# Kernel optimization log

Measured on AMD Instinct MI355X. Metric: run time of the kernel, lower is better.

Reference implementation:

```python
import jax, jax.numpy as jnp
import numpy as np

H, I, E, TOP_K = 2048, 5632, 8, 2


def _silu_mul_mlp(x, w_gate_up, w_down):
    # x: [T,H], w_gate_up: [H,2I], w_down: [I,H]
    gu = x @ w_gate_up
    g, u = jnp.split(gu, 2, axis=-1)
    return (jax.nn.silu(g) * u) @ w_down


def setup_inputs() -> dict:
    key = jax.random.key(0)
    ks = jax.random.split(key, 6)
    s = 0.02  # init scale for weights
    x = jax.random.normal(ks[0], (2, 1024, H), jnp.float32)
    gate_w = jax.random.normal(ks[1], (E, H), jnp.float32) * s
    base_gate_up = jax.random.normal(ks[2], (H, 2 * I), jnp.float32) * s
    base_down = jax.random.normal(ks[3], (I, H), jnp.float32) * s
    expert_gate_up = jax.random.normal(ks[4], (E, H, 2 * I), jnp.float32) * s
    expert_down = jax.random.normal(ks[5], (E, I, H), jnp.float32) * s
    return {"x": x, "gate_w": gate_w, "base_gate_up": base_gate_up,
            "base_down": base_down, "expert_gate_up": expert_gate_up,
            "expert_down": expert_down}


def reference(x, gate_w, base_gate_up, base_down, expert_gate_up, expert_down):
    B, S, Hd = x.shape
    xt = x.reshape(-1, Hd)  # [T,H]

    # Dense base MLP applied to every token (LlamaMLP with SiluAndMul)
    base_y = _silu_mul_mlp(xt, base_gate_up, base_down)  # [T,H]

    # Router: softmax in fp32, top-k, renormalize over selected experts
    logits = xt @ gate_w.T                              # [T,E]
    rw = jax.nn.softmax(logits.astype(jnp.float32), axis=-1)
    top_w, top_e = jax.lax.top_k(rw, TOP_K)             # [T,k]
    top_w = top_w / top_w.sum(axis=-1, keepdims=True)
    top_w = top_w.astype(x.dtype)

    # Combine weights per (token, expert): zero for unselected experts
    combine = (jax.nn.one_hot(top_e, E, dtype=x.dtype) * top_w[..., None]).sum(1)  # [T,E]

    # Expert MLPs (SwiGLU), vectorized over experts; masked-combine replaces
    # the original gather/scatter-add dispatch with identical math.
    gu = jnp.einsum('th,ehi->eti', xt, expert_gate_up)  # [E,T,2I]
    g, u = jnp.split(gu, 2, axis=-1)
    act = jax.nn.silu(g) * u                            # [E,T,I]
    out = jnp.einsum('eti,eih->eth', act, expert_down)  # [E,T,H]
    moe_y = jnp.einsum('eth,te->th', out, combine)      # [T,H]

    return (moe_y + base_y).reshape(B, S, Hd)
```

## Files before the change

### kernel.cpp

```cpp
#include <hip/hip_runtime.h>
#include <math.h>

#define H 2048
#define IDIM 5632
#define NE 8
#define TT 2048
#define LDW1 (2 * IDIM)
#define NK1 (H / 64)
#define NK2 (IDIM / 64)

typedef __bf16 bf16x8 __attribute__((ext_vector_type(8)));
typedef float f32x4 __attribute__((ext_vector_type(4)));

__device__ __forceinline__ unsigned short f2bf(float f) {
    unsigned int u = __builtin_bit_cast(unsigned int, f);
    u += 0x7FFFu + ((u >> 16) & 1u);
    return (unsigned short)(u >> 16);
}

__device__ __forceinline__ unsigned int pk2(float a, float b) {
    __bf16 x = (__bf16)a, y = (__bf16)b;
    unsigned short lo = __builtin_bit_cast(unsigned short, x);
    unsigned short hi = __builtin_bit_cast(unsigned short, y);
    return (unsigned int)lo | ((unsigned int)hi << 16);
}

__device__ __forceinline__ void gload_lds16(const void* g, void* l) {
    __builtin_amdgcn_global_load_lds(
        (const __attribute__((address_space(1))) void*)g,
        (__attribute__((address_space(3))) void*)l, 16, 0, 0);
}

#define PH_OPEN                                         \
    __builtin_amdgcn_s_barrier();                       \
    asm volatile("s_waitcnt lgkmcnt(0)" ::: "memory");  \
    __builtin_amdgcn_sched_barrier(0);                  \
    __builtin_amdgcn_s_setprio(1);
#define PH_CL                                           \
    __builtin_amdgcn_s_setprio(0);                      \
    __builtin_amdgcn_sched_barrier(0);                  \
    __builtin_amdgcn_s_barrier();

#define LDB_HALF(BR, kt, rlo)                                            \
    {                                                                    \
        _Pragma("unroll")                                                \
        for (int r_ = 0; r_ < 4; ++r_) {                                 \
            _Pragma("unroll")                                            \
            for (int j_ = 0; j_ < 4; ++j_)                               \
                BR[(rlo) + r_][j_] =                                     \
                    bp[j_][(size_t)((kt) * 64 + (rlo) + r_) * BST];      \
        }                                                                \
    }
#define WRB_HALF(BR, nb, jlo)                                            \
    {                                                                    \
        char* pbw_ = (char*)lds_b[nb];                                   \
        _Pragma("unroll")                                                \
        for (int j_ = (jlo); j_ < (jlo) + 2; ++j_) {                     \
            uint4 pk_;                                                   \
            pk_.x = pk2(BR[0][j_], BR[1][j_]);                           \
            pk_.y = pk2(BR[2][j_], BR[3][j_]);                           \
            pk_.z = pk2(BR[4][j_], BR[5][j_]);                           \
            pk_.w = pk2(BR[6][j_], BR[7][j_]);                           \
            *reinterpret_cast<uint4*>(pbw_ + bwaddr[j_]) = pk_;          \
        }                                                                \
    }

#define TILE_F(T, BRC, BRN, DO_STA, DO_LDB, DO_WR, VB)                   \
    {                                                                    \
        const int buf_ = (T) & 1, nbuf_ = buf_ ^ 1;                      \
        const char* pa_ = (const char*)lds_a[buf_];                      \
        const char* pb_ = (const char*)lds_b[buf_];                      \
        int slot0_ = (kq ^ lxor) << 4;                                   \
        int slot1_ = ((kq + 4) ^ lxor) << 4;                             \
        rdB(bfr, pb_, slot0_);                                           \
        rdA(a0, pa_, slot0_, 0);                                         \
        if (DO_STA) issueA((T) + 1, nbuf_);                              \
        if (DO_LDB) LDB_HALF(BRN, (T) + 2, 0)                            \
        PH_OPEN; mf16(a0, bfr, 0); PH_CL                                 \
        rdA(a1, pa_, slot0_, 1);                                         \
        if (DO_WR) WRB_HALF(BRC, nbuf_, 0)                               \
        PH_OPEN; mf16(a1, bfr, 1); PH_CL                                 \
        rdB(bfr, pb_, slot1_);                                           \
        rdA(a1, pa_, slot1_, 1);                                         \
        if (DO_LDB) LDB_HALF(BRN, (T) + 2, 4)                            \
        PH_OPEN; mf16(a1, bfr, 1); PH_CL                                 \
        rdA(a0, pa_, slot1_, 0);                                         \
        if (DO_WR) WRB_HALF(BRC, nbuf_, 2)                               \
        __builtin_amdgcn_s_barrier();                                    \
        asm volatile("s_waitcnt lgkmcnt(0)" ::: "memory");               \
        __builtin_amdgcn_sched_barrier(0);                               \
        __builtin_amdgcn_s_setprio(1);                                   \
        mf16(a0, bfr, 0);                                                \
        __builtin_amdgcn_s_setprio(0);                                   \
        __builtin_amdgcn_sched_barrier(0);                               \
        asm volatile("s_waitcnt vmcnt(" VB ")" ::: "memory");            \
        __builtin_amdgcn_sched_barrier(0);                               \
        __builtin_amdgcn_s_barrier();                                    \
        __builtin_amdgcn_sched_barrier(0);                               \
    }

__global__ void cvt_x_kernel(const float* __restrict__ x, unsigned short* __restrict__ xb) {
    int i = blockIdx.x * blockDim.x + threadIdx.x;
    float4 v = reinterpret_cast<const float4*>(x)[i];
    ushort4 o;
    o.x = f2bf(v.x); o.y = f2bf(v.y); o.z = f2bf(v.z); o.w = f2bf(v.w);
    reinterpret_cast<ushort4*>(xb)[i] = o;
}

__global__ void router_kernel(const float* __restrict__ x, const float* __restrict__ gw,
                              float* __restrict__ topw, int* __restrict__ cnt,
                              int* __restrict__ list) {
    int t = blockIdx.x;
    int lane = threadIdx.x;
    const float* xt = x + (size_t)t * H;
    double acc[NE];
#pragma unroll
    for (int e = 0; e < NE; ++e) acc[e] = 0.0;
    for (int h = lane; h < H; h += 64) {
        float xv = xt[h];
#pragma unroll
        for (int e = 0; e < NE; ++e) acc[e] += (double)xv * (double)gw[e * H + h];
    }
#pragma unroll
    for (int e = 0; e < NE; ++e) {
#pragma unroll
        for (int off = 32; off > 0; off >>= 1)
            acc[e] += __shfl_xor(acc[e], off, 64);
    }
    if (lane == 0) {
        double mx = acc[0];
#pragma unroll
        for (int e = 1; e < NE; ++e) mx = acc[e] > mx ? acc[e] : mx;
        double ex[NE], s = 0.0;
#pragma unroll
        for (int e = 0; e < NE; ++e) { ex[e] = exp(acc[e] - mx); s += ex[e]; }
        int e0 = 0; double b0 = ex[0];
#pragma unroll
        for (int e = 1; e < NE; ++e) if (ex[e] > b0) { b0 = ex[e]; e0 = e; }
        int e1 = -1; double b1 = -1.0;
#pragma unroll
        for (int e = 0; e < NE; ++e) if (e != e0 && ex[e] > b1) { b1 = ex[e]; e1 = e; }
        float p0 = (float)(b0 / s), p1 = (float)(b1 / s);
        float w0 = p0 / (p0 + p1), w1 = p1 / (p0 + p1);
        topw[t * 2 + 0] = w0;
        topw[t * 2 + 1] = w1;
        int pos0 = atomicAdd(&cnt[e0], 1); list[e0 * TT + pos0] = t * 2 + 0;
        int pos1 = atomicAdd(&cnt[e1], 1); list[e1 * TT + pos1] = t * 2 + 1;
    }
}

__global__ void setup_kernel(const int* __restrict__ cnt, int* __restrict__ tmap) {
    if (threadIdx.x == 0) {
        int a128 = 0, a256 = 0;
        tmap[0] = 0; tmap[20] = 0;
        for (int g = 0; g < 9; ++g) {
            int rows = (g == 0) ? TT : cnt[g - 1];
            tmap[10 + g] = rows;
            tmap[30 + g] = rows;
            a128 += (rows + 127) >> 7;
            a256 += (rows + 255) >> 8;
            tmap[g + 1] = a128;
            tmap[20 + g + 1] = a256;
        }
        tmap[19] = 0; tmap[39] = 0;
    }
}

__global__ __launch_bounds__(512)
void gemm1_kernel(const unsigned short* __restrict__ xb,
                  const float* __restrict__ base_gu,
                  const float* __restrict__ exp_gu,
                  const int* __restrict__ tmap,
                  const int* __restrict__ list,
                  unsigned short* __restrict__ actB,
                  unsigned short* __restrict__ actE) {
    __shared__ unsigned short lds_a[2][256 * 64];
    __shared__ unsigned short lds_b[2][256 * 64];
    __shared__ int s_arow[256];
    __shared__ int s_orow[256];
    __shared__ int sh[20];

    int tid = threadIdx.x;
    if (tid < 20) sh[tid] = tmap[20 + tid];
    __syncthreads();
    int bid = blockIdx.x;
    int virt = (bid & 7) * 176 + (bid >> 3);
    int jcol = virt >> 5;
    int rt = virt & 31;
    if (rt >= sh[9]) return;
    int g = 0;
    while (rt >= sh[g + 1]) ++g;
    int rows_g = sh[10 + g];
    int row0 = (rt - sh[g]) * 256;
    int n0a = jcol * 128;

    if (tid < 256) {
        int r = row0 + tid;
        int arow = 0, orow = 0;
        if (r < rows_g) {
            if (g == 0) { arow = r; orow = r; }
            else { int e = list[(g - 1) * TT + r]; arow = e >> 1; orow = e; }
        }
        s_arow[tid] = arow;
        s_orow[tid] = orow;
    }
    __syncthreads();

    const float* W = (g == 0) ? base_gu : (exp_gu + (size_t)(g - 1) * H * LDW1);
    unsigned short* actPtr = (g == 0) ? actB : actE;
    const size_t BST = LDW1;

    const unsigned short* asrc[4];
#pragma unroll
    for (int i = 0; i < 4; ++i) {
        int chunk = i * 512 + tid;
        int rl = chunk >> 3, kc = chunk & 7;
        asrc[i] = xb + (size_t)s_arow[rl] * H + ((kc ^ (rl & 7)) << 3);
    }
    int dstoff = (tid >> 6) * 1024;

    int ks = tid >> 6, cb = tid & 63;
    const float* bp[4];
    int bwaddr[4];
#pragma unroll
    for (int j = 0; j < 4; ++j) {
        int rl = cb + 64 * j;
        int wcol = (((rl >> 5) & 1) ? IDIM : 0) + n0a + ((rl >> 6) << 5) + (rl & 31);
        bp[j] = W + (size_t)(ks * 8) * LDW1 + wcol;
        bwaddr[j] = rl * 128 + ((ks ^ (cb & 7)) << 4);
    }

    auto issueA = [&](int kt, int buf) {
#pragma unroll
        for (int i = 0; i < 4; ++i)
            gload_lds16(asrc[i] + kt * 64, (char*)lds_a[buf] + i * 8192 + dstoff);
    };

    int wave = tid >> 6, lane = tid & 63;
    int wr = wave >> 2, wc = wave & 3;
    int arow0 = wr * 128 + (lane & 15);
    int bcol0 = wc * 64 + (lane & 15);
    int lxor = lane & 7;
    int kq = lane >> 4;

    f32x4 acc[8][4];
#pragma unroll
    for (int fm = 0; fm < 8; ++fm)
#pragma unroll
        for (int fn = 0; fn < 4; ++fn)
            acc[fm][fn] = (f32x4)(0.0f);

    bf16x8 a0[4], a1[4], bfr[4];
    auto rdA = [&](bf16x8* d, const char* pa, int slot, int fmh) {
#pragma unroll
        for (int i = 0; i < 4; ++i)
            d[i] = *reinterpret_cast<const bf16x8*>(pa + (arow0 + fmh * 64 + i * 16) * 128 + slot);
    };
    auto rdB = [&](bf16x8* d, const char* pb, int slot) {
#pragma unroll
        for (int fn = 0; fn < 4; ++fn)
            d[fn] = *reinterpret_cast<const bf16x8*>(pb + (bcol0 + fn * 16) * 128 + slot);
    };
    auto mf16 = [&](bf16x8* af, bf16x8* bf, int fmh) {
#pragma unroll
        for (int fn = 0; fn < 4; ++fn)
#pragma unroll
            for (int i = 0; i < 4; ++i)
                acc[fmh * 4 + i][fn] = __builtin_amdgcn_mfma_f32_16x16x32_bf16(
                    af[i], bf[fn], acc[fmh * 4 + i][fn], 0, 0, 0);
    };

    float brA[8][4], brB[8][4];

    issueA(0, 0);
    LDB_HALF(brB, 0, 0) LDB_HALF(brB, 0, 4)
    WRB_HALF(brB, 0, 0) WRB_HALF(brB, 0, 2)
    LDB_HALF(brA, 1, 0) LDB_HALF(brA, 1, 4)
    asm volatile("s_waitcnt vmcnt(32) lgkmcnt(0)" ::: "memory");
    __builtin_amdgcn_sched_barrier(0);
    __builtin_amdgcn_s_barrier();
    __builtin_amdgcn_sched_barrier(0);

    for (int t = 0; t + 3 < NK1; t += 2) {
        TILE_F(t, brA, brB, true, true, true, "32")
        TILE_F(t + 1, brB, brA, true, true, true, "32")
    }
    TILE_F(NK1 - 2, brA, brB, true, false, true, "0")
    TILE_F(NK1 - 1, brB, brA, false, false, false, "63")

    int cq = lane >> 4, cr = lane & 15;
#pragma unroll
    for (int fm = 0; fm < 8; ++fm) {
#pragma unroll
        for (int r = 0; r < 4; ++r) {
            int rloc = wr * 128 + fm * 16 + cq * 4 + r;
            if (row0 + rloc < rows_g) {
                size_t orow = (size_t)s_orow[rloc];
#pragma unroll
                for (int fn = 0; fn < 2; ++fn) {
                    float gv = acc[fm][fn][r];
                    float uv = acc[fm][fn + 2][r];
                    float sv = gv / (1.0f + __expf(-gv));
                    int col = n0a + wc * 32 + fn * 16 + cr;
                    actPtr[orow * IDIM + col] = f2bf(sv * uv);
                }
            }
        }
    }
}

__global__ __launch_bounds__(512)
void gemm2_kernel(const unsigned short* __restrict__ actB,
                  const unsigned short* __restrict__ actE,
                  const float* __restrict__ base_dn,
                  const float* __restrict__ exp_dn,
                  const int* __restrict__ tmap,
                  const int* __restrict__ list,
                  float* __restrict__ outB,
                  float* __restrict__ yslot) {
    __shared__ unsigned short lds_a[2][256 * 64];
    __shared__ unsigned short lds_b[2][256 * 64];
    __shared__ int s_row[256];
    __shared__ int sh[20];

    int tid = threadIdx.x;
    if (tid < 20) sh[tid] = tmap[20 + tid];
    __syncthreads();
    int bid = blockIdx.x;
    int virt = (bid & 7) * 32 + (bid >> 3);
    int jcol = virt >> 5;
    int rt = virt & 31;
    if (rt >= sh[9]) return;
    int g = 0;
    while (rt >= sh[g + 1]) ++g;
    int rows_g = sh[10 + g];
    int row0 = (rt - sh[g]) * 256;
    int n0 = jcol * 256;

    if (tid < 256) {
        int r = row0 + tid;
        int rowi = 0;
        if (r < rows_g) rowi = (g == 0) ? r : list[(g - 1) * TT + r];
        s_row[tid] = rowi;
    }
    __syncthreads();

    const unsigned short* abase = (g == 0) ? actB : actE;
    const float* W = (g == 0) ? base_dn : (exp_dn + (size_t)(g - 1) * IDIM * H);
    float* obase = (g == 0) ? outB : yslot;
    const size_t BST = H;

    const unsigned short* asrc[4];
#pragma unroll
    for (int i = 0; i < 4; ++i) {
        int chunk = i * 512 + tid;
        int rl = chunk >> 3, kc = chunk & 7;
        asrc[i] = abase + (size_t)s_row[rl] * IDIM + ((kc ^ (rl & 7)) << 3);
    }
    int dstoff = (tid >> 6) * 1024;

    int ks = tid >> 6, cb = tid & 63;
    const float* bp[4];
    int bwaddr[4];
#pragma unroll
    for (int j = 0; j < 4; ++j) {
        int rl = cb + 64 * j;
        bp[j] = W + (size_t)(ks * 8) * H + n0 + rl;
        bwaddr[j] = rl * 128 + ((ks ^ (cb & 7)) << 4);
    }

    auto issueA = [&](int kt, int buf) {
#pragma unroll
        for (int i = 0; i < 4; ++i)
            gload_lds16(asrc[i] + kt * 64, (char*)lds_a[buf] + i * 8192 + dstoff);
    };

    int wave = tid >> 6, lane = tid & 63;
    int wr = wave >> 2, wc = wave & 3;
    int arow0 = wr * 128 + (lane & 15);
    int bcol0 = wc * 64 + (lane & 15);
    int lxor = lane & 7;
    int kq = lane >> 4;

    f32x4 acc[8][4];
#pragma unroll
    for (int fm = 0; fm < 8; ++fm)
#pragma unroll
        for (int fn = 0; fn < 4; ++fn)
            acc[fm][fn] = (f32x4)(0.0f);

    bf16x8 a0[4], a1[4], bfr[4];
    auto rdA = [&](bf16x8* d, const char* pa, int slot, int fmh) {
#pragma unroll
        for (int i = 0; i < 4; ++i)
            d[i] = *reinterpret_cast<const bf16x8*>(pa + (arow0 + fmh * 64 + i * 16) * 128 + slot);
    };
    auto rdB = [&](bf16x8* d, const char* pb, int slot) {
#pragma unroll
        for (int fn = 0; fn < 4; ++fn)
            d[fn] = *reinterpret_cast<const bf16x8*>(pb + (bcol0 + fn * 16) * 128 + slot);
    };
    auto mf16 = [&](bf16x8* af, bf16x8* bf, int fmh) {
#pragma unroll
        for (int fn = 0; fn < 4; ++fn)
#pragma unroll
            for (int i = 0; i < 4; ++i)
                acc[fmh * 4 + i][fn] = __builtin_amdgcn_mfma_f32_16x16x32_bf16(
                    af[i], bf[fn], acc[fmh * 4 + i][fn], 0, 0, 0);
    };

    float brA[8][4], brB[8][4];

    issueA(0, 0);
    LDB_HALF(brB, 0, 0) LDB_HALF(brB, 0, 4)
    WRB_HALF(brB, 0, 0) WRB_HALF(brB, 0, 2)
    LDB_HALF(brA, 1, 0) LDB_HALF(brA, 1, 4)
    asm volatile("s_waitcnt vmcnt(32) lgkmcnt(0)" ::: "memory");
    __builtin_amdgcn_sched_barrier(0);
    __builtin_amdgcn_s_barrier();
    __builtin_amdgcn_sched_barrier(0);

    for (int t = 0; t + 3 < NK2; t += 2) {
        TILE_F(t, brA, brB, true, true, true, "32")
        TILE_F(t + 1, brB, brA, true, true, true, "32")
    }
    TILE_F(NK2 - 2, brA, brB, true, false, true, "0")
    TILE_F(NK2 - 1, brB, brA, false, false, false, "63")

    int cq = lane >> 4, cr = lane & 15;
#pragma unroll
    for (int fm = 0; fm < 8; ++fm) {
#pragma unroll
        for (int r = 0; r < 4; ++r) {
            int rloc = wr * 128 + fm * 16 + cq * 4 + r;
            if (row0 + rloc < rows_g) {
                size_t orow = (size_t)s_row[rloc];
#pragma unroll
                for (int fn = 0; fn < 4; ++fn) {
                    int col = n0 + wc * 64 + fn * 16 + cr;
                    obase[orow * H + col] = acc[fm][fn][r];
                }
            }
        }
    }
}

__global__ void combine_kernel(float* __restrict__ out, const float* __restrict__ yslot,
                               const float* __restrict__ topw) {
    int i = blockIdx.x * blockDim.x + threadIdx.x;
    int t = i >> 9;
    int c = (i & 511) << 2;
    float w0 = topw[t * 2], w1 = topw[t * 2 + 1];
    float4 y0 = *reinterpret_cast<const float4*>(yslot + ((size_t)(2 * t) * H + c));
    float4 y1 = *reinterpret_cast<const float4*>(yslot + ((size_t)(2 * t + 1) * H + c));
    float4* po = reinterpret_cast<float4*>(out + ((size_t)t * H + c));
    float4 o = *po;
    o.x += w0 * y0.x + w1 * y1.x;
    o.y += w0 * y0.y + w1 * y1.y;
    o.z += w0 * y0.z + w1 * y1.z;
    o.w += w0 * y0.w + w1 * y1.w;
    *po = o;
}

extern "C" void kernel_launch(void* const* d_in, const int* in_sizes, int n_in,
                              void* d_out, int out_size, void* d_ws, size_t ws_size,
                              hipStream_t stream) {
    const float* x   = (const float*)d_in[0];
    const float* gw  = (const float*)d_in[1];
    const float* bgu = (const float*)d_in[2];
    const float* bdn = (const float*)d_in[3];
    const float* egu = (const float*)d_in[4];
    const float* edn = (const float*)d_in[5];
    float* out = (float*)d_out;
    char* ws = (char*)d_ws;

    unsigned short* xb   = (unsigned short*)(ws + 0);
    unsigned short* actB = (unsigned short*)(ws + 8388608);
    unsigned short* actE = (unsigned short*)(ws + 31457280);
    float* yslot         = (float*)(ws + 77594624);
    float* topw          = (float*)(ws + 111149056);
    int* cnt             = (int*)(ws + 111165440);
    int* list            = (int*)(ws + 111165696);
    int* tmap            = (int*)(ws + 111231232);

    hipMemsetAsync(cnt, 0, NE * sizeof(int), stream);
    cvt_x_kernel<<<4096, 256, 0, stream>>>(x, xb);
    router_kernel<<<TT, 64, 0, stream>>>(x, gw, topw, cnt, list);
    setup_kernel<<<1, 64, 0, stream>>>(cnt, tmap);
    gemm1_kernel<<<1408, 512, 0, stream>>>(xb, bgu, egu, tmap, list, actB, actE);
    gemm2_kernel<<<256, 512, 0, stream>>>(actB, actE, bdn, edn, tmap, list, out, yslot);
    combine_kernel<<<4096, 256, 0, stream>>>(out, yslot, topw);
}
```

Baseline: 902.7 us.

## Switch GEMMs to producer/consumer warp-specialized pipeline with narrower N tiles

Both grouped GEMM kernels replace the hand-interleaved load/MFMA schedule with warp specialization: four waves stage A (direct-to-LDS) and fp32 B (converted to bf16) into double-buffered LDS, while four waves run MFMAs, synchronized once per k-step. The N tile is halved (128->64 in gemm1, 256->128 in gemm2) and grids are doubled accordingly. This simplifies scheduling and shrinks LDS, but halves the MFMA-issuing waves per block and doubles re-reads of the activation tile.

```diff
diff --git a/kernel.cpp b/kernel.cpp
--- a/kernel.cpp
+++ b/kernel.cpp
@@ -30,74 +30,6 @@
         (const __attribute__((address_space(1))) void*)g,
         (__attribute__((address_space(3))) void*)l, 16, 0, 0);
 }
-
-#define PH_OPEN                                         \
-    __builtin_amdgcn_s_barrier();                       \
-    asm volatile("s_waitcnt lgkmcnt(0)" ::: "memory");  \
-    __builtin_amdgcn_sched_barrier(0);                  \
-    __builtin_amdgcn_s_setprio(1);
-#define PH_CL                                           \
-    __builtin_amdgcn_s_setprio(0);                      \
-    __builtin_amdgcn_sched_barrier(0);                  \
-    __builtin_amdgcn_s_barrier();
-
-#define LDB_HALF(BR, kt, rlo)                                            \
-    {                                                                    \
-        _Pragma("unroll")                                                \
-        for (int r_ = 0; r_ < 4; ++r_) {                                 \
-            _Pragma("unroll")                                            \
-            for (int j_ = 0; j_ < 4; ++j_)                               \
-                BR[(rlo) + r_][j_] =                                     \
-                    bp[j_][(size_t)((kt) * 64 + (rlo) + r_) * BST];      \
-        }                                                                \
-    }
-#define WRB_HALF(BR, nb, jlo)                                            \
-    {                                                                    \
-        char* pbw_ = (char*)lds_b[nb];                                   \
-        _Pragma("unroll")                                                \
-        for (int j_ = (jlo); j_ < (jlo) + 2; ++j_) {                     \
-            uint4 pk_;                                                   \
-            pk_.x = pk2(BR[0][j_], BR[1][j_]);                           \
-            pk_.y = pk2(BR[2][j_], BR[3][j_]);                           \
-            pk_.z = pk2(BR[4][j_], BR[5][j_]);                           \
-            pk_.w = pk2(BR[6][j_], BR[7][j_]);                           \
-            *reinterpret_cast<uint4*>(pbw_ + bwaddr[j_]) = pk_;          \
-        }                                                                \
-    }
-
-#define TILE_F(T, BRC, BRN, DO_STA, DO_LDB, DO_WR, VB)                   \
-    {                                                                    \
-        const int buf_ = (T) & 1, nbuf_ = buf_ ^ 1;                      \
-        const char* pa_ = (const char*)lds_a[buf_];                      \
-        const char* pb_ = (const char*)lds_b[buf_];                      \
-        int slot0_ = (kq ^ lxor) << 4;                                   \
-        int slot1_ = ((kq + 4) ^ lxor) << 4;                             \
-        rdB(bfr, pb_, slot0_);                                           \
-        rdA(a0, pa_, slot0_, 0);                                         \
-        if (DO_STA) issueA((T) + 1, nbuf_);                              \
-        if (DO_LDB) LDB_HALF(BRN, (T) + 2, 0)                            \
-        PH_OPEN; mf16(a0, bfr, 0); PH_CL                                 \
-        rdA(a1, pa_, slot0_, 1);                                         \
-        if (DO_WR) WRB_HALF(BRC, nbuf_, 0)                               \
-        PH_OPEN; mf16(a1, bfr, 1); PH_CL                                 \
-        rdB(bfr, pb_, slot1_);                                           \
-        rdA(a1, pa_, slot1_, 1);                                         \
-        if (DO_LDB) LDB_HALF(BRN, (T) + 2, 4)                            \
-        PH_OPEN; mf16(a1, bfr, 1); PH_CL                                 \
-        rdA(a0, pa_, slot1_, 0);                                         \
-        if (DO_WR) WRB_HALF(BRC, nbuf_, 2)                               \
-        __builtin_amdgcn_s_barrier();                                    \
-        asm volatile("s_waitcnt lgkmcnt(0)" ::: "memory");               \
-        __builtin_amdgcn_sched_barrier(0);                               \
-        __builtin_amdgcn_s_setprio(1);                                   \
-        mf16(a0, bfr, 0);                                                \
-        __builtin_amdgcn_s_setprio(0);                                   \
-        __builtin_amdgcn_sched_barrier(0);                               \
-        asm volatile("s_waitcnt vmcnt(" VB ")" ::: "memory");            \
-        __builtin_amdgcn_sched_barrier(0);                               \
-        __builtin_amdgcn_s_barrier();                                    \
-        __builtin_amdgcn_sched_barrier(0);                               \
-    }
 
 __global__ void cvt_x_kernel(const float* __restrict__ x, unsigned short* __restrict__ xb) {
     int i = blockIdx.x * blockDim.x + threadIdx.x;
@@ -175,7 +107,7 @@
                   unsigned short* __restrict__ actB,
                   unsigned short* __restrict__ actE) {
     __shared__ unsigned short lds_a[2][256 * 64];
-    __shared__ unsigned short lds_b[2][256 * 64];
+    __shared__ unsigned short lds_b[2][128 * 64];
     __shared__ int s_arow[256];
     __shared__ int s_orow[256];
     __shared__ int sh[20];
@@ -184,7 +116,7 @@
     if (tid < 20) sh[tid] = tmap[20 + tid];
     __syncthreads();
     int bid = blockIdx.x;
-    int virt = (bid & 7) * 176 + (bid >> 3);
+    int virt = (bid & 7) * 352 + (bid >> 3);
     int jcol = virt >> 5;
     int rt = virt & 31;
     if (rt >= sh[9]) return;
@@ -192,7 +124,7 @@
     while (rt >= sh[g + 1]) ++g;
     int rows_g = sh[10 + g];
     int row0 = (rt - sh[g]) * 256;
-    int n0a = jcol * 128;
+    int n0a = jcol * 64;
 
     if (tid < 256) {
         int r = row0 + tid;
@@ -208,36 +140,57 @@
 
     const float* W = (g == 0) ? base_gu : (exp_gu + (size_t)(g - 1) * H * LDW1);
     unsigned short* actPtr = (g == 0) ? actB : actE;
-    const size_t BST = LDW1;
-
-    const unsigned short* asrc[4];
-#pragma unroll
-    for (int i = 0; i < 4; ++i) {
-        int chunk = i * 512 + tid;
-        int rl = chunk >> 3, kc = chunk & 7;
-        asrc[i] = xb + (size_t)s_arow[rl] * H + ((kc ^ (rl & 7)) << 3);
-    }
-    int dstoff = (tid >> 6) * 1024;
-
-    int ks = tid >> 6, cb = tid & 63;
-    const float* bp[4];
-    int bwaddr[4];
-#pragma unroll
-    for (int j = 0; j < 4; ++j) {
-        int rl = cb + 64 * j;
-        int wcol = (((rl >> 5) & 1) ? IDIM : 0) + n0a + ((rl >> 6) << 5) + (rl & 31);
-        bp[j] = W + (size_t)(ks * 8) * LDW1 + wcol;
-        bwaddr[j] = rl * 128 + ((ks ^ (cb & 7)) << 4);
-    }
-
-    auto issueA = [&](int kt, int buf) {
-#pragma unroll
-        for (int i = 0; i < 4; ++i)
-            gload_lds16(asrc[i] + kt * 64, (char*)lds_a[buf] + i * 8192 + dstoff);
+
+    int wave = tid >> 6, lane = tid & 63;
+    bool producer = (wave >= 4);
+    int ptid = tid & 255;
+
+    const unsigned short* asrc[8];
+#pragma unroll
+    for (int i = 0; i < 8; ++i) {
+        int chunk = i * 256 + ptid;
+        int sA = chunk >> 3, kc = chunk & 7;
+        asrc[i] = xb + (size_t)s_arow[sA] * H + ((kc ^ (sA & 7)) << 3);
+    }
+    int dstoffA = (ptid >> 6) * 1024;
+
+    int cb = ptid & 63, ks = ptid >> 6;
+    int wcol0 = (((cb >> 5) & 1) ? IDIM : 0) + n0a + (cb & 31);
+    const float* bp0 = W + (size_t)(ks * 16) * LDW1 + wcol0;
+    const float* bp1 = bp0 + 32;
+    int bwa[4];
+    bwa[0] = cb * 128 + (((2 * ks) ^ (cb & 7)) << 4);
+    bwa[1] = cb * 128 + (((2 * ks + 1) ^ (cb & 7)) << 4);
+    bwa[2] = bwa[0] + 64 * 128;
+    bwa[3] = bwa[1] + 64 * 128;
+
+    auto stageTile = [&](int kt, int nb) {
+#pragma unroll
+        for (int i = 0; i < 8; ++i)
+            gload_lds16(asrc[i] + kt * 64, (char*)lds_a[nb] + i * 4096 + dstoffA);
+        float v0[16], v1[16];
+#pragma unroll
+        for (int r = 0; r < 16; ++r) {
+            v0[r] = bp0[(size_t)(kt * 64 + r) * LDW1];
+            v1[r] = bp1[(size_t)(kt * 64 + r) * LDW1];
+        }
+        char* pbw = (char*)lds_b[nb];
+        uint4 pk;
+        pk.x = pk2(v0[0], v0[1]);  pk.y = pk2(v0[2], v0[3]);
+        pk.z = pk2(v0[4], v0[5]);  pk.w = pk2(v0[6], v0[7]);
+        *reinterpret_cast<uint4*>(pbw + bwa[0]) = pk;
+        pk.x = pk2(v0[8], v0[9]);  pk.y = pk2(v0[10], v0[11]);
+        pk.z = pk2(v0[12], v0[13]); pk.w = pk2(v0[14], v0[15]);
+        *reinterpret_cast<uint4*>(pbw + bwa[1]) = pk;
+        pk.x = pk2(v1[0], v1[1]);  pk.y = pk2(v1[2], v1[3]);
+        pk.z = pk2(v1[4], v1[5]);  pk.w = pk2(v1[6], v1[7]);
+        *reinterpret_cast<uint4*>(pbw + bwa[2]) = pk;
+        pk.x = pk2(v1[8], v1[9]);  pk.y = pk2(v1[10], v1[11]);
+        pk.z = pk2(v1[12], v1[13]); pk.w = pk2(v1[14], v1[15]);
+        *reinterpret_cast<uint4*>(pbw + bwa[3]) = pk;
     };
 
-    int wave = tid >> 6, lane = tid & 63;
-    int wr = wave >> 2, wc = wave & 3;
+    int wr = (wave >> 1) & 1, wc = wave & 1;
     int arow0 = wr * 128 + (lane & 15);
     int bcol0 = wc * 64 + (lane & 15);
     int lxor = lane & 7;
@@ -250,59 +203,54 @@
         for (int fn = 0; fn < 4; ++fn)
             acc[fm][fn] = (f32x4)(0.0f);
 
-    bf16x8 a0[4], a1[4], bfr[4];
-    auto rdA = [&](bf16x8* d, const char* pa, int slot, int fmh) {
-#pragma unroll
-        for (int i = 0; i < 4; ++i)
-            d[i] = *reinterpret_cast<const bf16x8*>(pa + (arow0 + fmh * 64 + i * 16) * 128 + slot);
+    auto compute = [&](int buf) {
+        const char* pa = (const char*)lds_a[buf];
+        const char* pb = (const char*)lds_b[buf];
+#pragma unroll
+        for (int kh = 0; kh < 2; ++kh) {
+            int slot = ((kq + kh * 4) ^ lxor) << 4;
+            bf16x8 bF[4], aF[8];
+#pragma unroll
+            for (int fn = 0; fn < 4; ++fn)
+                bF[fn] = *reinterpret_cast<const bf16x8*>(pb + (bcol0 + fn * 16) * 128 + slot);
+#pragma unroll
+            for (int i = 0; i < 8; ++i)
+                aF[i] = *reinterpret_cast<const bf16x8*>(pa + (arow0 + i * 16) * 128 + slot);
+#pragma unroll
+            for (int i = 0; i < 8; ++i)
+#pragma unroll
+                for (int fn = 0; fn < 4; ++fn)
+                    acc[i][fn] = __builtin_amdgcn_mfma_f32_16x16x32_bf16(
+                        aF[i], bF[fn], acc[i][fn], 0, 0, 0);
+        }
     };
-    auto rdB = [&](bf16x8* d, const char* pb, int slot) {
-#pragma unroll
-        for (int fn = 0; fn < 4; ++fn)
-            d[fn] = *reinterpret_cast<const bf16x8*>(pb + (bcol0 + fn * 16) * 128 + slot);
-    };
-    auto mf16 = [&](bf16x8* af, bf16x8* bf, int fmh) {
-#pragma unroll
-        for (int fn = 0; fn < 4; ++fn)
-#pragma unroll
-            for (int i = 0; i < 4; ++i)
-                acc[fmh * 4 + i][fn] = __builtin_amdgcn_mfma_f32_16x16x32_bf16(
-                    af[i], bf[fn], acc[fmh * 4 + i][fn], 0, 0, 0);
-    };
-
-    float brA[8][4], brB[8][4];
-
-    issueA(0, 0);
-    LDB_HALF(brB, 0, 0) LDB_HALF(brB, 0, 4)
-    WRB_HALF(brB, 0, 0) WRB_HALF(brB, 0, 2)
-    LDB_HALF(brA, 1, 0) LDB_HALF(brA, 1, 4)
-    asm volatile("s_waitcnt vmcnt(32) lgkmcnt(0)" ::: "memory");
-    __builtin_amdgcn_sched_barrier(0);
-    __builtin_amdgcn_s_barrier();
-    __builtin_amdgcn_sched_barrier(0);
-
-    for (int t = 0; t + 3 < NK1; t += 2) {
-        TILE_F(t, brA, brB, true, true, true, "32")
-        TILE_F(t + 1, brB, brA, true, true, true, "32")
-    }
-    TILE_F(NK1 - 2, brA, brB, true, false, true, "0")
-    TILE_F(NK1 - 1, brB, brA, false, false, false, "63")
-
-    int cq = lane >> 4, cr = lane & 15;
-#pragma unroll
-    for (int fm = 0; fm < 8; ++fm) {
-#pragma unroll
-        for (int r = 0; r < 4; ++r) {
-            int rloc = wr * 128 + fm * 16 + cq * 4 + r;
-            if (row0 + rloc < rows_g) {
-                size_t orow = (size_t)s_orow[rloc];
-#pragma unroll
-                for (int fn = 0; fn < 2; ++fn) {
-                    float gv = acc[fm][fn][r];
-                    float uv = acc[fm][fn + 2][r];
-                    float sv = gv / (1.0f + __expf(-gv));
-                    int col = n0a + wc * 32 + fn * 16 + cr;
-                    actPtr[orow * IDIM + col] = f2bf(sv * uv);
+
+    if (producer) stageTile(0, 0);
+    __syncthreads();
+    for (int t = 0; t < NK1; ++t) {
+        int buf = t & 1;
+        if (!producer) compute(buf);
+        else if (t + 1 < NK1) stageTile(t + 1, buf ^ 1);
+        __syncthreads();
+    }
+
+    if (!producer) {
+        int cq = lane >> 4, cr = lane & 15;
+#pragma unroll
+        for (int fm = 0; fm < 8; ++fm) {
+#pragma unroll
+            for (int r = 0; r < 4; ++r) {
+                int rloc = wr * 128 + fm * 16 + cq * 4 + r;
+                if (row0 + rloc < rows_g) {
+                    size_t orow = (size_t)s_orow[rloc];
+#pragma unroll
+                    for (int fn = 0; fn < 2; ++fn) {
+                        float gv = acc[fm][fn][r];
+                        float uv = acc[fm][fn + 2][r];
+                        float sv = gv / (1.0f + __expf(-gv));
+                        int col = n0a + wc * 32 + fn * 16 + cr;
+                        actPtr[orow * IDIM + col] = f2bf(sv * uv);
+                    }
                 }
             }
         }
@@ -319,7 +267,7 @@
                   float* __restrict__ outB,
                   float* __restrict__ yslot) {
     __shared__ unsigned short lds_a[2][256 * 64];
-    __shared__ unsigned short lds_b[2][256 * 64];
+    __shared__ unsigned short lds_b[2][128 * 64];
     __shared__ int s_row[256];
     __shared__ int sh[20];
 
@@ -327,7 +275,7 @@
     if (tid < 20) sh[tid] = tmap[20 + tid];
     __syncthreads();
     int bid = blockIdx.x;
-    int virt = (bid & 7) * 32 + (bid >> 3);
+    int virt = (bid & 7) * 64 + (bid >> 3);
     int jcol = virt >> 5;
     int rt = virt & 31;
     if (rt >= sh[9]) return;
@@ -335,7 +283,7 @@
     while (rt >= sh[g + 1]) ++g;
     int rows_g = sh[10 + g];
     int row0 = (rt - sh[g]) * 256;
-    int n0 = jcol * 256;
+    int n0 = jcol * 128;
 
     if (tid < 256) {
         int r = row0 + tid;
@@ -348,35 +296,56 @@
     const unsigned short* abase = (g == 0) ? actB : actE;
     const float* W = (g == 0) ? base_dn : (exp_dn + (size_t)(g - 1) * IDIM * H);
     float* obase = (g == 0) ? outB : yslot;
-    const size_t BST = H;
-
-    const unsigned short* asrc[4];
-#pragma unroll
-    for (int i = 0; i < 4; ++i) {
-        int chunk = i * 512 + tid;
-        int rl = chunk >> 3, kc = chunk & 7;
-        asrc[i] = abase + (size_t)s_row[rl] * IDIM + ((kc ^ (rl & 7)) << 3);
-    }
-    int dstoff = (tid >> 6) * 1024;
-
-    int ks = tid >> 6, cb = tid & 63;
-    const float* bp[4];
-    int bwaddr[4];
-#pragma unroll
-    for (int j = 0; j < 4; ++j) {
-        int rl = cb + 64 * j;
-        bp[j] = W + (size_t)(ks * 8) * H + n0 + rl;
-        bwaddr[j] = rl * 128 + ((ks ^ (cb & 7)) << 4);
-    }
-
-    auto issueA = [&](int kt, int buf) {
-#pragma unroll
-        for (int i = 0; i < 4; ++i)
-            gload_lds16(asrc[i] + kt * 64, (char*)lds_a[buf] + i * 8192 + dstoff);
+
+    int wave = tid >> 6, lane = tid & 63;
+    bool producer = (wave >= 4);
+    int ptid = tid & 255;
+
+    const unsigned short* asrc[8];
+#pragma unroll
+    for (int i = 0; i < 8; ++i) {
+        int chunk = i * 256 + ptid;
+        int sA = chunk >> 3, kc = chunk & 7;
+        asrc[i] = abase + (size_t)s_row[sA] * IDIM + ((kc ^ (sA & 7)) << 3);
+    }
+    int dstoffA = (ptid >> 6) * 1024;
+
+    int cb = ptid & 63, ks = ptid >> 6;
+    const float* bp0 = W + (size_t)(ks * 16) * H + n0 + cb;
+    const float* bp1 = bp0 + 64;
+    int bwa[4];
+    bwa[0] = cb * 128 + (((2 * ks) ^ (cb & 7)) << 4);
+    bwa[1] = cb * 128 + (((2 * ks + 1) ^ (cb & 7)) << 4);
+    bwa[2] = bwa[0] + 64 * 128;
+    bwa[3] = bwa[1] + 64 * 128;
+
+    auto stageTile = [&](int kt, int nb) {
+#pragma unroll
+        for (int i = 0; i < 8; ++i)
+            gload_lds16(asrc[i] + kt * 64, (char*)lds_a[nb] + i * 4096 + dstoffA);
+        float v0[16], v1[16];
+#pragma unroll
+        for (int r = 0; r < 16; ++r) {
+            v0[r] = bp0[(size_t)(kt * 64 + r) * H];
+            v1[r] = bp1[(size_t)(kt * 64 + r) * H];
+        }
+        char* pbw = (char*)lds_b[nb];
+        uint4 pk;
+        pk.x = pk2(v0[0], v0[1]);  pk.y = pk2(v0[2], v0[3]);
+        pk.z = pk2(v0[4], v0[5]);  pk.w = pk2(v0[6], v0[7]);
+        *reinterpret_cast<uint4*>(pbw + bwa[0]) = pk;
+        pk.x = pk2(v0[8], v0[9]);  pk.y = pk2(v0[10], v0[11]);
+        pk.z = pk2(v0[12], v0[13]); pk.w = pk2(v0[14], v0[15]);
+        *reinterpret_cast<uint4*>(pbw + bwa[1]) = pk;
+        pk.x = pk2(v1[0], v1[1]);  pk.y = pk2(v1[2], v1[3]);
+        pk.z = pk2(v1[4], v1[5]);  pk.w = pk2(v1[6], v1[7]);
+        *reinterpret_cast<uint4*>(pbw + bwa[2]) = pk;
+        pk.x = pk2(v1[8], v1[9]);  pk.y = pk2(v1[10], v1[11]);
+        pk.z = pk2(v1[12], v1[13]); pk.w = pk2(v1[14], v1[15]);
+        *reinterpret_cast<uint4*>(pbw + bwa[3]) = pk;
     };
 
-    int wave = tid >> 6, lane = tid & 63;
-    int wr = wave >> 2, wc = wave & 3;
+    int wr = (wave >> 1) & 1, wc = wave & 1;
     int arow0 = wr * 128 + (lane & 15);
     int bcol0 = wc * 64 + (lane & 15);
     int lxor = lane & 7;
@@ -389,56 +358,51 @@
         for (int fn = 0; fn < 4; ++fn)
             acc[fm][fn] = (f32x4)(0.0f);
 
-    bf16x8 a0[4], a1[4], bfr[4];
-    auto rdA = [&](bf16x8* d, const char* pa, int slot, int fmh) {
-#pragma unroll
-        for (int i = 0; i < 4; ++i)
-            d[i] = *reinterpret_cast<const bf16x8*>(pa + (arow0 + fmh * 64 + i * 16) * 128 + slot);
+    auto compute = [&](int buf) {
+        const char* pa = (const char*)lds_a[buf];
+        const char* pb = (const char*)lds_b[buf];
+#pragma unroll
+        for (int kh = 0; kh < 2; ++kh) {
+            int slot = ((kq + kh * 4) ^ lxor) << 4;
+            bf16x8 bF[4], aF[8];
+#pragma unroll
+            for (int fn = 0; fn < 4; ++fn)
+                bF[fn] = *reinterpret_cast<const bf16x8*>(pb + (bcol0 + fn * 16) * 128 + slot);
+#pragma unroll
+            for (int i = 0; i < 8; ++i)
+                aF[i] = *reinterpret_cast<const bf16x8*>(pa + (arow0 + i * 16) * 128 + slot);
+#pragma unroll
+            for (int i = 0; i < 8; ++i)
+#pragma unroll
+                for (int fn = 0; fn < 4; ++fn)
+                    acc[i][fn] = __builtin_amdgcn_mfma_f32_16x16x32_bf16(
+                        aF[i], bF[fn], acc[i][fn], 0, 0, 0);
+        }
     };
-    auto rdB = [&](bf16x8* d, const char* pb, int slot) {
-#pragma unroll
-        for (int fn = 0; fn < 4; ++fn)
-            d[fn] = *reinterpret_cast<const bf16x8*>(pb + (bcol0 + fn * 16) * 128 + slot);
-    };
-    auto mf16 = [&](bf16x8* af, bf16x8* bf, int fmh) {
-#pragma unroll
-        for (int fn = 0; fn < 4; ++fn)
-#pragma unroll
-            for (int i = 0; i < 4; ++i)
-                acc[fmh * 4 + i][fn] = __builtin_amdgcn_mfma_f32_16x16x32_bf16(
-                    af[i], bf[fn], acc[fmh * 4 + i][fn], 0, 0, 0);
-    };
-
-    float brA[8][4], brB[8][4];
-
-    issueA(0, 0);
-    LDB_HALF(brB, 0, 0) LDB_HALF(brB, 0, 4)
-    WRB_HALF(brB, 0, 0) WRB_HALF(brB, 0, 2)
-    LDB_HALF(brA, 1, 0) LDB_HALF(brA, 1, 4)
-    asm volatile("s_waitcnt vmcnt(32) lgkmcnt(0)" ::: "memory");
-    __builtin_amdgcn_sched_barrier(0);
-    __builtin_amdgcn_s_barrier();
-    __builtin_amdgcn_sched_barrier(0);
-
-    for (int t = 0; t + 3 < NK2; t += 2) {
-        TILE_F(t, brA, brB, true, true, true, "32")
-        TILE_F(t + 1, brB, brA, true, true, true, "32")
-    }
-    TILE_F(NK2 - 2, brA, brB, true, false, true, "0")
-    TILE_F(NK2 - 1, brB, brA, false, false, false, "63")
-
-    int cq = lane >> 4, cr = lane & 15;
-#pragma unroll
-    for (int fm = 0; fm < 8; ++fm) {
-#pragma unroll
-        for (int r = 0; r < 4; ++r) {
-            int rloc = wr * 128 + fm * 16 + cq * 4 + r;
-            if (row0 + rloc < rows_g) {
-                size_t orow = (size_t)s_row[rloc];
-#pragma unroll
-                for (int fn = 0; fn < 4; ++fn) {
-                    int col = n0 + wc * 64 + fn * 16 + cr;
-                    obase[orow * H + col] = acc[fm][fn][r];
+
+    if (producer) stageTile(0, 0);
+    __syncthreads();
+    for (int t = 0; t < NK2; ++t) {
+        int buf = t & 1;
+        if (!producer) compute(buf);
+        else if (t + 1 < NK2) stageTile(t + 1, buf ^ 1);
+        __syncthreads();
+    }
+
+    if (!producer) {
+        int cq = lane >> 4, cr = lane & 15;
+#pragma unroll
+        for (int fm = 0; fm < 8; ++fm) {
+#pragma unroll
+            for (int r = 0; r < 4; ++r) {
+                int rloc = wr * 128 + fm * 16 + cq * 4 + r;
+                if (row0 + rloc < rows_g) {
+                    size_t orow = (size_t)s_row[rloc];
+#pragma unroll
+                    for (int fn = 0; fn < 4; ++fn) {
+                        int col = n0 + wc * 64 + fn * 16 + cr;
+                        obase[orow * H + col] = acc[fm][fn][r];
+                    }
                 }
             }
         }
@@ -487,7 +451,7 @@
     cvt_x_kernel<<<4096, 256, 0, stream>>>(x, xb);
     router_kernel<<<TT, 64, 0, stream>>>(x, gw, topw, cnt, list);
     setup_kernel<<<1, 64, 0, stream>>>(cnt, tmap);
-    gemm1_kernel<<<1408, 512, 0, stream>>>(xb, bgu, egu, tmap, list, actB, actE);
-    gemm2_kernel<<<256, 512, 0, stream>>>(actB, actE, bdn, edn, tmap, list, out, yslot);
+    gemm1_kernel<<<2816, 512, 0, stream>>>(xb, bgu, egu, tmap, list, actB, actE);
+    gemm2_kernel<<<512, 512, 0, stream>>>(actB, actE, bdn, edn, tmap, list, out, yslot);
     combine_kernel<<<4096, 256, 0, stream>>>(out, yslot, topw);
 }
```

After: 1.004 ms. 11.3% more time.

## Replace fine-grained phased MFMA schedule with simpler per-tile compute pipeline

Applied to the files above, without the earlier changes.

Removes the hand-interleaved phase schedule, in which LDS reads, global B loads, B writes and MFMA groups were split into quarters separated by barriers and priority changes. Each K tile now issues the next A async load and the B prefetch, runs a compute lambda that reads all fragments per K half and issues the MFMAs, then writes B and synchronises once. This cuts barrier count per tile and leaves instruction scheduling to the compiler. In exchange it loses explicit overlap between LDS reads and MFMAs and raises register pressure, since 8 A fragments are held at once. The tail also waits for a stricter vmcnt before the final tile.

```diff
diff --git a/kernel.cpp b/kernel.cpp
--- a/kernel.cpp
+++ b/kernel.cpp
@@ -31,31 +31,20 @@
         (__attribute__((address_space(3))) void*)l, 16, 0, 0);
 }
 
-#define PH_OPEN                                         \
-    __builtin_amdgcn_s_barrier();                       \
-    asm volatile("s_waitcnt lgkmcnt(0)" ::: "memory");  \
-    __builtin_amdgcn_sched_barrier(0);                  \
-    __builtin_amdgcn_s_setprio(1);
-#define PH_CL                                           \
-    __builtin_amdgcn_s_setprio(0);                      \
-    __builtin_amdgcn_sched_barrier(0);                  \
-    __builtin_amdgcn_s_barrier();
-
-#define LDB_HALF(BR, kt, rlo)                                            \
+#define LDB_T(BR, KT)                                                    \
     {                                                                    \
         _Pragma("unroll")                                                \
-        for (int r_ = 0; r_ < 4; ++r_) {                                 \
+        for (int r_ = 0; r_ < 8; ++r_) {                                 \
             _Pragma("unroll")                                            \
             for (int j_ = 0; j_ < 4; ++j_)                               \
-                BR[(rlo) + r_][j_] =                                     \
-                    bp[j_][(size_t)((kt) * 64 + (rlo) + r_) * BST];      \
+                BR[r_][j_] = bp[j_][(size_t)((KT) * 64 + r_) * BST];     \
         }                                                                \
     }
-#define WRB_HALF(BR, nb, jlo)                                            \
+#define WRB_T(BR, NB)                                                    \
     {                                                                    \
-        char* pbw_ = (char*)lds_b[nb];                                   \
+        char* pbw_ = (char*)lds_b[NB];                                   \
         _Pragma("unroll")                                                \
-        for (int j_ = (jlo); j_ < (jlo) + 2; ++j_) {                     \
+        for (int j_ = 0; j_ < 4; ++j_) {                                 \
             uint4 pk_;                                                   \
             pk_.x = pk2(BR[0][j_], BR[1][j_]);                           \
             pk_.y = pk2(BR[2][j_], BR[3][j_]);                           \
@@ -65,35 +54,14 @@
         }                                                                \
     }
 
-#define TILE_F(T, BRC, BRN, DO_STA, DO_LDB, DO_WR, VB)                   \
+#define TILE_S(T, BRC, BRN, LD2, VB)                                     \
     {                                                                    \
         const int buf_ = (T) & 1, nbuf_ = buf_ ^ 1;                      \
-        const char* pa_ = (const char*)lds_a[buf_];                      \
-        const char* pb_ = (const char*)lds_b[buf_];                      \
-        int slot0_ = (kq ^ lxor) << 4;                                   \
-        int slot1_ = ((kq + 4) ^ lxor) << 4;                             \
-        rdB(bfr, pb_, slot0_);                                           \
-        rdA(a0, pa_, slot0_, 0);                                         \
-        if (DO_STA) issueA((T) + 1, nbuf_);                              \
-        if (DO_LDB) LDB_HALF(BRN, (T) + 2, 0)                            \
-        PH_OPEN; mf16(a0, bfr, 0); PH_CL                                 \
-        rdA(a1, pa_, slot0_, 1);                                         \
-        if (DO_WR) WRB_HALF(BRC, nbuf_, 0)                               \
-        PH_OPEN; mf16(a1, bfr, 1); PH_CL                                 \
-        rdB(bfr, pb_, slot1_);                                           \
-        rdA(a1, pa_, slot1_, 1);                                         \
-        if (DO_LDB) LDB_HALF(BRN, (T) + 2, 4)                            \
-        PH_OPEN; mf16(a1, bfr, 1); PH_CL                                 \
-        rdA(a0, pa_, slot1_, 0);                                         \
-        if (DO_WR) WRB_HALF(BRC, nbuf_, 2)                               \
-        __builtin_amdgcn_s_barrier();                                    \
-        asm volatile("s_waitcnt lgkmcnt(0)" ::: "memory");               \
-        __builtin_amdgcn_sched_barrier(0);                               \
-        __builtin_amdgcn_s_setprio(1);                                   \
-        mf16(a0, bfr, 0);                                                \
-        __builtin_amdgcn_s_setprio(0);                                   \
-        __builtin_amdgcn_sched_barrier(0);                               \
-        asm volatile("s_waitcnt vmcnt(" VB ")" ::: "memory");            \
+        issueA((T) + 1, nbuf_);                                          \
+        if (LD2) LDB_T(BRN, (T) + 2)                                     \
+        compute(buf_);                                                   \
+        WRB_T(BRC, nbuf_)                                                \
+        asm volatile("s_waitcnt vmcnt(" VB ") lgkmcnt(0)" ::: "memory"); \
         __builtin_amdgcn_sched_barrier(0);                               \
         __builtin_amdgcn_s_barrier();                                    \
         __builtin_amdgcn_sched_barrier(0);                               \
@@ -250,43 +218,47 @@
         for (int fn = 0; fn < 4; ++fn)
             acc[fm][fn] = (f32x4)(0.0f);
 
-    bf16x8 a0[4], a1[4], bfr[4];
-    auto rdA = [&](bf16x8* d, const char* pa, int slot, int fmh) {
-#pragma unroll
-        for (int i = 0; i < 4; ++i)
-            d[i] = *reinterpret_cast<const bf16x8*>(pa + (arow0 + fmh * 64 + i * 16) * 128 + slot);
+    auto compute = [&](int buf) {
+        const char* pa = (const char*)lds_a[buf];
+        const char* pb = (const char*)lds_b[buf];
+        __builtin_amdgcn_s_setprio(1);
+#pragma unroll
+        for (int kh = 0; kh < 2; ++kh) {
+            int slot = ((kq + kh * 4) ^ lxor) << 4;
+            bf16x8 bF[4], aF[8];
+#pragma unroll
+            for (int fn = 0; fn < 4; ++fn)
+                bF[fn] = *reinterpret_cast<const bf16x8*>(pb + (bcol0 + fn * 16) * 128 + slot);
+#pragma unroll
+            for (int i = 0; i < 8; ++i)
+                aF[i] = *reinterpret_cast<const bf16x8*>(pa + (arow0 + i * 16) * 128 + slot);
+#pragma unroll
+            for (int i = 0; i < 8; ++i)
+#pragma unroll
+                for (int fn = 0; fn < 4; ++fn)
+                    acc[i][fn] = __builtin_amdgcn_mfma_f32_16x16x32_bf16(
+                        aF[i], bF[fn], acc[i][fn], 0, 0, 0);
+        }
+        __builtin_amdgcn_s_setprio(0);
     };
-    auto rdB = [&](bf16x8* d, const char* pb, int slot) {
-#pragma unroll
-        for (int fn = 0; fn < 4; ++fn)
-            d[fn] = *reinterpret_cast<const bf16x8*>(pb + (bcol0 + fn * 16) * 128 + slot);
-    };
-    auto mf16 = [&](bf16x8* af, bf16x8* bf, int fmh) {
-#pragma unroll
-        for (int fn = 0; fn < 4; ++fn)
-#pragma unroll
-            for (int i = 0; i < 4; ++i)
-                acc[fmh * 4 + i][fn] = __builtin_amdgcn_mfma_f32_16x16x32_bf16(
-                    af[i], bf[fn], acc[fmh * 4 + i][fn], 0, 0, 0);
-    };
 
     float brA[8][4], brB[8][4];
 
     issueA(0, 0);
-    LDB_HALF(brB, 0, 0) LDB_HALF(brB, 0, 4)
-    WRB_HALF(brB, 0, 0) WRB_HALF(brB, 0, 2)
-    LDB_HALF(brA, 1, 0) LDB_HALF(brA, 1, 4)
-    asm volatile("s_waitcnt vmcnt(32) lgkmcnt(0)" ::: "memory");
+    LDB_T(brB, 0)
+    WRB_T(brB, 0)
+    LDB_T(brA, 1)
+    asm volatile("s_waitcnt lgkmcnt(0)" ::: "memory");
     __builtin_amdgcn_sched_barrier(0);
     __builtin_amdgcn_s_barrier();
     __builtin_amdgcn_sched_barrier(0);
 
     for (int t = 0; t + 3 < NK1; t += 2) {
-        TILE_F(t, brA, brB, true, true, true, "32")
-        TILE_F(t + 1, brB, brA, true, true, true, "32")
-    }
-    TILE_F(NK1 - 2, brA, brB, true, false, true, "0")
-    TILE_F(NK1 - 1, brB, brA, false, false, false, "63")
+        TILE_S(t, brA, brB, true, "32")
+        TILE_S(t + 1, brB, brA, true, "32")
+    }
+    TILE_S(NK1 - 2, brA, brB, false, "0")
+    compute((NK1 - 1) & 1);
 
     int cq = lane >> 4, cr = lane & 15;
 #pragma unroll
@@ -389,43 +361,47 @@
         for (int fn = 0; fn < 4; ++fn)
             acc[fm][fn] = (f32x4)(0.0f);
 
-    bf16x8 a0[4], a1[4], bfr[4];
-    auto rdA = [&](bf16x8* d, const char* pa, int slot, int fmh) {
-#pragma unroll
-        for (int i = 0; i < 4; ++i)
-            d[i] = *reinterpret_cast<const bf16x8*>(pa + (arow0 + fmh * 64 + i * 16) * 128 + slot);
+    auto compute = [&](int buf) {
+        const char* pa = (const char*)lds_a[buf];
+        const char* pb = (const char*)lds_b[buf];
+        __builtin_amdgcn_s_setprio(1);
+#pragma unroll
+        for (int kh = 0; kh < 2; ++kh) {
+            int slot = ((kq + kh * 4) ^ lxor) << 4;
+            bf16x8 bF[4], aF[8];
+#pragma unroll
+            for (int fn = 0; fn < 4; ++fn)
+                bF[fn] = *reinterpret_cast<const bf16x8*>(pb + (bcol0 + fn * 16) * 128 + slot);
+#pragma unroll
+            for (int i = 0; i < 8; ++i)
+                aF[i] = *reinterpret_cast<const bf16x8*>(pa + (arow0 + i * 16) * 128 + slot);
+#pragma unroll
+            for (int i = 0; i < 8; ++i)
+#pragma unroll
+                for (int fn = 0; fn < 4; ++fn)
+                    acc[i][fn] = __builtin_amdgcn_mfma_f32_16x16x32_bf16(
+                        aF[i], bF[fn], acc[i][fn], 0, 0, 0);
+        }
+        __builtin_amdgcn_s_setprio(0);
     };
-    auto rdB = [&](bf16x8* d, const char* pb, int slot) {
-#pragma unroll
-        for (int fn = 0; fn < 4; ++fn)
-            d[fn] = *reinterpret_cast<const bf16x8*>(pb + (bcol0 + fn * 16) * 128 + slot);
-    };
-    auto mf16 = [&](bf16x8* af, bf16x8* bf, int fmh) {
-#pragma unroll
-        for (int fn = 0; fn < 4; ++fn)
-#pragma unroll
-            for (int i = 0; i < 4; ++i)
-                acc[fmh * 4 + i][fn] = __builtin_amdgcn_mfma_f32_16x16x32_bf16(
-                    af[i], bf[fn], acc[fmh * 4 + i][fn], 0, 0, 0);
-    };
 
     float brA[8][4], brB[8][4];
 
     issueA(0, 0);
-    LDB_HALF(brB, 0, 0) LDB_HALF(brB, 0, 4)
-    WRB_HALF(brB, 0, 0) WRB_HALF(brB, 0, 2)
-    LDB_HALF(brA, 1, 0) LDB_HALF(brA, 1, 4)
-    asm volatile("s_waitcnt vmcnt(32) lgkmcnt(0)" ::: "memory");
+    LDB_T(brB, 0)
+    WRB_T(brB, 0)
+    LDB_T(brA, 1)
+    asm volatile("s_waitcnt lgkmcnt(0)" ::: "memory");
     __builtin_amdgcn_sched_barrier(0);
     __builtin_amdgcn_s_barrier();
     __builtin_amdgcn_sched_barrier(0);
 
     for (int t = 0; t + 3 < NK2; t += 2) {
-        TILE_F(t, brA, brB, true, true, true, "32")
-        TILE_F(t + 1, brB, brA, true, true, true, "32")
-    }
-    TILE_F(NK2 - 2, brA, brB, true, false, true, "0")
-    TILE_F(NK2 - 1, brB, brA, false, false, false, "63")
+        TILE_S(t, brA, brB, true, "32")
+        TILE_S(t + 1, brB, brA, true, "32")
+    }
+    TILE_S(NK2 - 2, brA, brB, false, "0")
+    compute((NK2 - 1) & 1);
 
     int cq = lane >> 4, cr = lane & 15;
 #pragma unroll
```

New measurement: 2.513 ms. 178% more time.
